# Kernel optimization log

Hardware: AMD Instinct MI355X
Metric: run time of the kernel (lower is better)

Reference implementation:

```python
import jax, jax.numpy as jnp
import numpy as np

N, E, F_IN, H, C = 50000, 800000, 128, 128, 64


def setup_inputs() -> dict:
    key = jax.random.key(0)
    ks = jax.random.split(key, 10)
    s = lambda f: np.float32(1.0 / np.sqrt(f))
    return {
        "x": jax.random.normal(ks[0], (N, F_IN), jnp.float32),
        "edge_index": jax.random.randint(ks[1], (2, E), 0, N, dtype=jnp.int64),
        # SAGEConv1: lin_l (on aggregated neighbors, with bias) + lin_r (on root, no bias)
        "W1l": jax.random.normal(ks[2], (F_IN, H), jnp.float32) * s(F_IN),
        "b1l": jnp.zeros((H,), jnp.float32),
        "W1r": jax.random.normal(ks[3], (F_IN, H), jnp.float32) * s(F_IN),
        # SAGEConv2
        "W2l": jax.random.normal(ks[4], (H, C), jnp.float32) * s(H),
        "b2l": jnp.zeros((C,), jnp.float32),
        "W2r": jax.random.normal(ks[5], (H, C), jnp.float32) * s(H),
        # GCNConv
        "Wg": jax.random.normal(ks[6], (C, C), jnp.float32) * s(C),
        "bg": jnp.zeros((C,), jnp.float32),
    }


def sage_conv(x, edge_index, Wl, bl, Wr):
    # PyG SAGEConv (mean aggr): out = lin_l(mean_{j in N(i)} x_j) + lin_r(x_i)
    n = x.shape[0]
    src, dst = edge_index[0], edge_index[1]
    agg = jax.ops.segment_sum(x[src], dst, num_segments=n)  # [N, F]
    cnt = jax.ops.segment_sum(jnp.ones((src.shape[0],), x.dtype), dst, num_segments=n)
    mean = agg / jnp.maximum(cnt, 1.0)[:, None]
    return mean @ Wl + bl + x @ Wr


def gcn_conv(x, edge_index, W, b):
    # PyG GCNConv: add self loops, symmetric normalization D^-1/2 A D^-1/2
    n = x.shape[0]
    loop = jnp.arange(n, dtype=edge_index.dtype)
    src = jnp.concatenate([edge_index[0], loop])
    dst = jnp.concatenate([edge_index[1], loop])
    deg = jax.ops.segment_sum(jnp.ones((src.shape[0],), x.dtype), dst, num_segments=n)
    dinv = jnp.where(deg > 0, jax.lax.rsqrt(jnp.maximum(deg, 1e-12)), 0.0)
    norm = dinv[src] * dinv[dst]  # [E+N]
    xw = x @ W
    out = jax.ops.segment_sum(xw[src] * norm[:, None], dst, num_segments=n)
    return out + b


def reference(x, edge_index, W1l, b1l, W1r, W2l, b2l, W2r, Wg, bg):
    h = jax.nn.relu(sage_conv(x, edge_index, W1l, b1l, W1r))
    # dropout is identity in eval mode
    h = sage_conv(h, edge_index, W2l, b2l, W2r)
    h = jax.nn.softmax(h, axis=1)  # activate='softmax'
    return gcn_conv(h, edge_index, Wg, bg)
```

## Files before the change

kernel.cpp:

```cpp
#include <hip/hip_runtime.h>
#include <hip/hip_fp16.h>
#include <math.h>


typedef __attribute__((ext_vector_type(8))) short bf16x8;
typedef __attribute__((ext_vector_type(4))) float f32x4;
typedef __attribute__((ext_vector_type(2))) float f32v2;

__device__ inline unsigned short f32_bf16_hi(float f) {
    unsigned int u = __builtin_bit_cast(unsigned int, f);
    u = (u + 0x7FFFu + ((u >> 16) & 1u)) >> 16;
    return (unsigned short)u;
}
__device__ inline float bf16_to_f32(unsigned short h) {
    unsigned int u = ((unsigned int)h) << 16;
    return __builtin_bit_cast(float, u);
}

union H8 { float4 f4; __half2 h[4]; };

__device__ inline void dec16(uint4 u, float* a0, float* a1) {
    f32v2 x0 = __builtin_amdgcn_cvt_pk_f32_fp8(u.x, false);
    f32v2 x1 = __builtin_amdgcn_cvt_pk_f32_fp8(u.x, true);
    f32v2 y0 = __builtin_amdgcn_cvt_pk_f32_fp8(u.y, false);
    f32v2 y1 = __builtin_amdgcn_cvt_pk_f32_fp8(u.y, true);
    a0[0] += x0[0]; a0[1] += x0[1]; a0[2] += x1[0]; a0[3] += x1[1];
    a0[4] += y0[0]; a0[5] += y0[1]; a0[6] += y1[0]; a0[7] += y1[1];
    f32v2 z0 = __builtin_amdgcn_cvt_pk_f32_fp8(u.z, false);
    f32v2 z1 = __builtin_amdgcn_cvt_pk_f32_fp8(u.z, true);
    f32v2 w0 = __builtin_amdgcn_cvt_pk_f32_fp8(u.w, false);
    f32v2 w1 = __builtin_amdgcn_cvt_pk_f32_fp8(u.w, true);
    a1[0] += z0[0]; a1[1] += z0[1]; a1[2] += z1[0]; a1[3] += z1[1];
    a1[4] += w0[0]; a1[5] += w0[1]; a1[6] += w1[0]; a1[7] += w1[1];
}

__global__ void count_kernel(const int* __restrict__ dst, int* __restrict__ off,
                             int E, int NB, int BK) {
    __shared__ int hist[256];
    int t = threadIdx.x;
    hist[t] = 0;
    __syncthreads();
    int base = blockIdx.x * 8192;
    for (int i = t; i < 8192; i += 256) {
        int e = base + i;
        if (e < E) atomicAdd(&hist[dst[e] >> 8], 1);
    }
    __syncthreads();
    if (t < BK) off[1 + t * NB + blockIdx.x] = hist[t];
    if (blockIdx.x == 0 && t == 0) off[0] = 0;
}

__global__ void scan_reduce_kernel(const int* __restrict__ data, int* __restrict__ bsum, int n) {
    __shared__ int red[256];
    int t = threadIdx.x;
    int base = blockIdx.x * 2048 + t * 8;
    int s = 0;
    if (base + 8 <= n) {
        int4 a = *(const int4*)(data + base);
        int4 b = *(const int4*)(data + base + 4);
        s = a.x + a.y + a.z + a.w + b.x + b.y + b.z + b.w;
    } else {
        for (int i = 0; i < 8; ++i)
            if (base + i < n) s += data[base + i];
    }
    red[t] = s;
    __syncthreads();
    for (int off = 128; off > 0; off >>= 1) {
        if (t < off) red[t] += red[t + off];
        __syncthreads();
    }
    if (t == 0) bsum[blockIdx.x] = red[0];
}

__global__ void scan_offsets_kernel(int* __restrict__ bsum, int B) {
    if (threadIdx.x == 0 && blockIdx.x == 0) {
        int run = 0;
        for (int i = 0; i < B; ++i) { int v = bsum[i]; bsum[i] = run; run += v; }
    }
}

__global__ void scan_final_kernel(int* __restrict__ data, const int* __restrict__ bsum, int n) {
    __shared__ int tsum[256];
    int t = threadIdx.x;
    int base = blockIdx.x * 2048 + t * 8;
    int v[8];
    int s = 0;
#pragma unroll
    for (int i = 0; i < 8; ++i) {
        v[i] = (base + i < n) ? data[base + i] : 0;
        s += v[i];
    }
    tsum[t] = s;
    for (int off = 1; off < 256; off <<= 1) {
        __syncthreads();
        int u = (t >= off) ? tsum[t - off] : 0;
        __syncthreads();
        tsum[t] += u;
    }
    __syncthreads();
    int run = bsum[blockIdx.x] + tsum[t] - s;
#pragma unroll
    for (int i = 0; i < 8; ++i) {
        run += v[i];
        if (base + i < n) data[base + i] = run;
    }
}

__global__ void partition_kernel(const int* __restrict__ src, const int* __restrict__ dst,
                                 const int* __restrict__ off, unsigned* __restrict__ ebuf,
                                 int E, int NB, int BK) {
    __shared__ int cur[256];
    int t = threadIdx.x;
    if (t < BK) cur[t] = off[t * NB + blockIdx.x];
    __syncthreads();
    int base = blockIdx.x * 8192;
    for (int i = t; i < 8192; i += 256) {
        int e = base + i;
        if (e < E) {
            int d = dst[e];
            int pos = atomicAdd(&cur[d >> 8], 1);
            ebuf[pos] = ((unsigned)src[e] << 8) | (unsigned)(d & 255);
        }
    }
}

__global__ void finalize_kernel(const unsigned* __restrict__ ebuf, const int* __restrict__ off,
                                int* __restrict__ col, int* __restrict__ rowptr,
                                float* __restrict__ dinv, int N, int NB, int E) {
    __shared__ int hist[256], scn[256], cur[256];
    int b = blockIdx.x, t = threadIdx.x;
    int base = off[b * NB];
    int end  = off[(b + 1) * NB];
    int M = end - base;
    hist[t] = 0;
    __syncthreads();
    for (int i = t; i < M; i += 256) atomicAdd(&hist[ebuf[base + i] & 255u], 1);
    __syncthreads();
    scn[t] = hist[t];
    for (int o = 1; o < 256; o <<= 1) {
        __syncthreads();
        int u = (t >= o) ? scn[t - o] : 0;
        __syncthreads();
        scn[t] += u;
    }
    __syncthreads();
    int excl = scn[t] - hist[t];
    int node = b * 256 + t;
    if (node < N) {
        rowptr[node] = base + excl;
        dinv[node] = rsqrtf((float)(hist[t] + 1));
    }
    if (b == 0 && t == 0) rowptr[N] = E;
    cur[t] = base + excl;
    __syncthreads();
    for (int i = t; i < M; i += 256) {
        unsigned w = ebuf[base + i];
        int pos = atomicAdd(&cur[w & 255u], 1);
        col[pos] = (int)(w >> 8);
    }
}

__global__ void packw_kernel(const float* __restrict__ W1l, const float* __restrict__ W1r,
                             const float* __restrict__ W2l, const float* __restrict__ W2r,
                             const float* __restrict__ Wg,
                             unsigned short* __restrict__ p1h, unsigned short* __restrict__ p1l,
                             unsigned short* __restrict__ p2h, unsigned short* __restrict__ p2l,
                             unsigned short* __restrict__ p3h, unsigned short* __restrict__ p3l) {
    int which = blockIdx.y;
    const float* W;
    unsigned short *hi, *lo;
    int K, Mp, colOff, T;
    if (which == 0)      { W = W1l; hi = p1h; lo = p1l; K = 128; Mp = 128; colOff = 0;   T = 16; }
    else if (which == 1) { W = W1r; hi = p1h; lo = p1l; K = 128; Mp = 128; colOff = 128; T = 16; }
    else if (which == 2) { W = W2l; hi = p2h; lo = p2l; K = 128; Mp = 64;  colOff = 0;   T = 8;  }
    else if (which == 3) { W = W2r; hi = p2h; lo = p2l; K = 128; Mp = 64;  colOff = 64;  T = 8;  }
    else                 { W = Wg;  hi = p3h; lo = p3l; K = 64;  Mp = 64;  colOff = 0;   T = 4;  }
    int idx = blockIdx.x * blockDim.x + threadIdx.x;
    if (idx >= K * Mp) return;
    int k = idx / Mp, m = idx % Mp;
    float w = W[(size_t)k * Mp + m];
    int colI = colOff + m;
    int s = k >> 5, kk = k & 31, qq = kk >> 3, j = kk & 7;
    int tt = colI >> 4, n = colI & 15;
    int lane = qq * 16 + n;
    size_t pos = ((size_t)(s * T + tt) * 64 + lane) * 8 + j;
    unsigned short h = f32_bf16_hi(w);
    hi[pos] = h;
    lo[pos] = f32_bf16_hi(w - bf16_to_f32(h));
}

__launch_bounds__(256)
__global__ void gemm1_kernel(const float* __restrict__ A,
                             const unsigned short* __restrict__ Whi,
                             const unsigned short* __restrict__ Wlo,
                             unsigned char* __restrict__ outA8, __half* __restrict__ outB, int N) {
    constexpr int Ttot = 16, TB = 8;
    __shared__ __align__(16) unsigned char pk[4][16][128];
    const int lane = threadIdx.x & 63;
    const int wave = threadIdx.x >> 6;
    const int m = lane & 15, q = lane >> 4;
    const int t0 = blockIdx.y * TB;
    const int row0 = blockIdx.x * 64 + wave * 16;
    int arow = row0 + m;
    if (arow >= N) arow = N - 1;
    const float* ap = A + (size_t)arow * 128 + q * 8;

    float av[4][8];
#pragma unroll
    for (int s = 0; s < 4; ++s) {
        *(float4*)(av[s])     = *(const float4*)(ap + s * 32);
        *(float4*)(av[s] + 4) = *(const float4*)(ap + s * 32 + 4);
    }
    bf16x8 ahi[4], alo[4];
#pragma unroll
    for (int s = 0; s < 4; ++s)
#pragma unroll
        for (int i = 0; i < 8; ++i) {
            unsigned short h = f32_bf16_hi(av[s][i]);
            ahi[s][i] = (short)h;
            alo[s][i] = (short)f32_bf16_hi(av[s][i] - bf16_to_f32(h));
        }

    f32x4 acc[TB];
#pragma unroll
    for (int t = 0; t < TB; ++t) acc[t] = (f32x4)(0.f);
    const bf16x8* whp = (const bf16x8*)Whi;
    const bf16x8* wlp = (const bf16x8*)Wlo;
#pragma unroll
    for (int s = 0; s < 4; ++s) {
        const int base = (s * Ttot + t0) * 64 + lane;
#pragma unroll
        for (int t = 0; t < TB; ++t) {
            bf16x8 wh = whp[base + t * 64];
            bf16x8 wl = wlp[base + t * 64];
            acc[t] = __builtin_amdgcn_mfma_f32_16x16x32_bf16(ahi[s], wh, acc[t], 0, 0, 0);
            acc[t] = __builtin_amdgcn_mfma_f32_16x16x32_bf16(alo[s], wh, acc[t], 0, 0, 0);
            acc[t] = __builtin_amdgcn_mfma_f32_16x16x32_bf16(ahi[s], wl, acc[t], 0, 0, 0);
        }
    }

    if (blockIdx.y == 0) {
#pragma unroll
        for (int r = 0; r < 4; ++r) {
            int row = q * 4 + r;
            int sw = (row & 3) << 5;
#pragma unroll
            for (int t = 0; t < 8; t += 2) {
                int w = __builtin_amdgcn_cvt_pk_fp8_f32(acc[t][r], acc[t + 1][r], 0, false);
                int off = (t >> 1) * 8 + (m & 7);
                int c0 = ((2 * t + (m >> 3)) & 3) * 32 + off;
                int c1 = ((2 * t + 2 + (m >> 3)) & 3) * 32 + off;
                pk[wave][row][c0 ^ sw] = (unsigned char)(w & 0xff);
                pk[wave][row][c1 ^ sw] = (unsigned char)((w >> 8) & 0xff);
            }
        }
        __syncthreads();
        int rr = lane >> 2, qt = lane & 3;
        int grow = row0 + rr;
        if (grow < N) {
            const unsigned char* srcp = &pk[wave][rr][(qt ^ (rr & 3)) * 32];
            uint4 v0 = *(const uint4*)(srcp);
            uint4 v1 = *(const uint4*)(srcp + 16);
            *(uint4*)(outA8 + (size_t)grow * 128 + qt * 32) = v0;
            *(uint4*)(outA8 + (size_t)grow * 128 + qt * 32 + 16) = v1;
        }
    } else {
#pragma unroll
        for (int r = 0; r < 4; ++r) {
            int row = row0 + q * 4 + r;
            if (row < N) {
#pragma unroll
                for (int t = 0; t < TB; ++t) {
                    int c = (t0 + t) * 16 + m - 128;
                    outB[(size_t)row * 128 + c] = __float2half(acc[t][r]);
                }
            }
        }
    }
}

__launch_bounds__(256)
__global__ void sage2_fused_kernel(const unsigned char* __restrict__ p8, const __half* __restrict__ q16,
                                   const int* __restrict__ rowptr, const int* __restrict__ col,
                                   const float* __restrict__ b1l,
                                   const unsigned short* __restrict__ Whi,
                                   const unsigned short* __restrict__ Wlo,
                                   __half* __restrict__ r16, __half* __restrict__ s16, int N) {
    __shared__ float part[4][64][16];
    const int lane = threadIdx.x & 63;
    const int w = threadIdx.x >> 6;
    const int m = lane & 15, q = lane >> 4;
    const int row0 = blockIdx.x * 16;
    int node = row0 + m;
    int nclamp = (node < N) ? node : (N - 1);
    int sAll = rowptr[nclamp];
    int eAll = (node < N) ? rowptr[nclamp + 1] : sAll;
    int deg  = eAll - sAll;
    int sIdx = sAll + ((deg * w) >> 2);
    int eIdx = sAll + ((deg * (w + 1)) >> 2);

    float acc[4][8];
#pragma unroll
    for (int s = 0; s < 4; ++s)
#pragma unroll
        for (int i = 0; i < 8; ++i) acc[s][i] = 0.f;

    const unsigned char* pb = p8 + q * 32;
    int ptr = sIdx;
    for (; ptr + 4 <= eIdx; ptr += 4) {
        int j0 = col[ptr], j1 = col[ptr + 1], j2 = col[ptr + 2], j3 = col[ptr + 3];
        uint4 uA[4], uB[4];
        uA[0] = *(const uint4*)(pb + (size_t)j0 * 128);
        uB[0] = *(const uint4*)(pb + (size_t)j0 * 128 + 16);
        uA[1] = *(const uint4*)(pb + (size_t)j1 * 128);
        uB[1] = *(const uint4*)(pb + (size_t)j1 * 128 + 16);
        uA[2] = *(const uint4*)(pb + (size_t)j2 * 128);
        uB[2] = *(const uint4*)(pb + (size_t)j2 * 128 + 16);
        uA[3] = *(const uint4*)(pb + (size_t)j3 * 128);
        uB[3] = *(const uint4*)(pb + (size_t)j3 * 128 + 16);
#pragma unroll
        for (int e = 0; e < 4; ++e) {
            dec16(uA[e], acc[0], acc[1]);
            dec16(uB[e], acc[2], acc[3]);
        }
    }
    for (; ptr < eIdx; ++ptr) {
        int j0 = col[ptr];
        uint4 uA = *(const uint4*)(pb + (size_t)j0 * 128);
        uint4 uB = *(const uint4*)(pb + (size_t)j0 * 128 + 16);
        dec16(uA, acc[0], acc[1]);
        dec16(uB, acc[2], acc[3]);
    }

    float* ap = &acc[0][0];
    const int swz = lane & 3;
#pragma unroll
    for (int c = 0; c < 2; ++c) {
        if (c) __syncthreads();
#pragma unroll
        for (int sl = 0; sl < 4; ++sl)
            *(float4*)&part[w][lane][(sl ^ swz) * 4] =
                *(const float4*)(ap + (c * 4 + sl) * 4);
        __syncthreads();
#pragma unroll
        for (int p = 1; p < 4; ++p) {
#pragma unroll
            for (int sl = 0; sl < 4; ++sl) {
                float4 pv = *(const float4*)&part[w ^ p][lane][(sl ^ swz) * 4];
                int g = (c * 4 + sl) * 4;
                ap[g]     += pv.x;
                ap[g + 1] += pv.y;
                ap[g + 2] += pv.z;
                ap[g + 3] += pv.w;
            }
        }
    }

    float inv = 1.0f / fmaxf((float)deg, 1.0f);
    bf16x8 ahi[4], alo[4];
#pragma unroll
    for (int s = 0; s < 4; ++s) {
        H8 qv;
        qv.f4 = *(const float4*)(q16 + (size_t)nclamp * 128 + s * 32 + q * 8);
        float bv[8];
        *(float4*)(bv)     = *(const float4*)(b1l + s * 32 + q * 8);
        *(float4*)(bv + 4) = *(const float4*)(b1l + s * 32 + q * 8 + 4);
#pragma unroll
        for (int i = 0; i < 8; ++i) {
            float qf = __half2float(((const __half*)&qv)[i]);
            float h = fmaxf(acc[s][i] * inv + qf + bv[i], 0.f);
            unsigned short hb = f32_bf16_hi(h);
            ahi[s][i] = (short)hb;
            alo[s][i] = (short)f32_bf16_hi(h - bf16_to_f32(hb));
        }
    }

    f32x4 accm[2];
#pragma unroll
    for (int t = 0; t < 2; ++t) accm[t] = (f32x4)(0.f);
    const bf16x8* whp = (const bf16x8*)Whi;
    const bf16x8* wlp = (const bf16x8*)Wlo;
#pragma unroll
    for (int s = 0; s < 4; ++s) {
        const int base = (s * 8 + 2 * w) * 64 + lane;
#pragma unroll
        for (int t = 0; t < 2; ++t) {
            bf16x8 wh = whp[base + t * 64];
            bf16x8 wl = wlp[base + t * 64];
            accm[t] = __builtin_amdgcn_mfma_f32_16x16x32_bf16(ahi[s], wh, accm[t], 0, 0, 0);
            accm[t] = __builtin_amdgcn_mfma_f32_16x16x32_bf16(alo[s], wh, accm[t], 0, 0, 0);
            accm[t] = __builtin_amdgcn_mfma_f32_16x16x32_bf16(ahi[s], wl, accm[t], 0, 0, 0);
        }
    }
    __half* op = (w >= 2) ? s16 : r16;
#pragma unroll
    for (int r = 0; r < 4; ++r) {
        int row = row0 + q * 4 + r;
        if (row < N) {
#pragma unroll
            for (int t = 0; t < 2; ++t) {
                int c = ((2 * w + t) * 16 + m) & 63;
                op[(size_t)row * 64 + c] = __float2half(accm[t][r]);
            }
        }
    }
}

__launch_bounds__(256)
__global__ void gcn_prep_fused_kernel(const __half* __restrict__ r16, const __half* __restrict__ s16,
                                      const int* __restrict__ rowptr, const int* __restrict__ col,
                                      const float* __restrict__ b2l,
                                      const unsigned short* __restrict__ Whi,
                                      const unsigned short* __restrict__ Wlo,
                                      const float* __restrict__ dinv,
                                      __half* __restrict__ tp16, int N) {
    __shared__ float part[4][64][16];
    const int lane = threadIdx.x & 63;
    const int w = threadIdx.x >> 6;
    const int m = lane & 15, q = lane >> 4;
    const int row0 = blockIdx.x * 16;
    int node = row0 + m;
    int nclamp = (node < N) ? node : (N - 1);
    int sAll = rowptr[nclamp];
    int eAll = (node < N) ? rowptr[nclamp + 1] : sAll;
    int deg  = eAll - sAll;
    int sIdx = sAll + ((deg * w) >> 2);
    int eIdx = sAll + ((deg * (w + 1)) >> 2);

    float acc[2][8];
#pragma unroll
    for (int s = 0; s < 2; ++s)
#pragma unroll
        for (int i = 0; i < 8; ++i) acc[s][i] = 0.f;

    const __half* rb = r16 + q * 8;
    int ptr = sIdx;
    for (; ptr + 4 <= eIdx; ptr += 4) {
        int j0 = col[ptr], j1 = col[ptr + 1], j2 = col[ptr + 2], j3 = col[ptr + 3];
        H8 u[4][2];
#pragma unroll
        for (int s = 0; s < 2; ++s) {
            u[0][s].f4 = *(const float4*)(rb + (size_t)j0 * 64 + s * 32);
            u[1][s].f4 = *(const float4*)(rb + (size_t)j1 * 64 + s * 32);
            u[2][s].f4 = *(const float4*)(rb + (size_t)j2 * 64 + s * 32);
            u[3][s].f4 = *(const float4*)(rb + (size_t)j3 * 64 + s * 32);
        }
#pragma unroll
        for (int s = 0; s < 2; ++s)
#pragma unroll
            for (int k = 0; k < 4; ++k) {
                float2 f0 = __half22float2(u[0][s].h[k]);
                float2 f1 = __half22float2(u[1][s].h[k]);
                float2 f2 = __half22float2(u[2][s].h[k]);
                float2 f3 = __half22float2(u[3][s].h[k]);
                acc[s][2 * k]     += (f0.x + f1.x) + (f2.x + f3.x);
                acc[s][2 * k + 1] += (f0.y + f1.y) + (f2.y + f3.y);
            }
    }
    for (; ptr < eIdx; ++ptr) {
        int j0 = col[ptr];
#pragma unroll
        for (int s = 0; s < 2; ++s) {
            H8 u0;
            u0.f4 = *(const float4*)(rb + (size_t)j0 * 64 + s * 32);
#pragma unroll
            for (int k = 0; k < 4; ++k) {
                float2 f0 = __half22float2(u0.h[k]);
                acc[s][2 * k]     += f0.x;
                acc[s][2 * k + 1] += f0.y;
            }
        }
    }

    float* ap = &acc[0][0];
    const int swz = lane & 3;
#pragma unroll
    for (int sl = 0; sl < 4; ++sl)
        *(float4*)&part[w][lane][(sl ^ swz) * 4] = *(const float4*)(ap + sl * 4);
    __syncthreads();
#pragma unroll
    for (int p = 1; p < 4; ++p) {
#pragma unroll
        for (int sl = 0; sl < 4; ++sl) {
            float4 pv = *(const float4*)&part[w ^ p][lane][(sl ^ swz) * 4];
            ap[sl * 4]     += pv.x;
            ap[sl * 4 + 1] += pv.y;
            ap[sl * 4 + 2] += pv.z;
            ap[sl * 4 + 3] += pv.w;
        }
    }

    float inv = 1.0f / fmaxf((float)deg, 1.0f);
    float v[2][8];
    float mx = -1e30f;
#pragma unroll
    for (int s = 0; s < 2; ++s) {
        H8 sv;
        sv.f4 = *(const float4*)(s16 + (size_t)nclamp * 64 + s * 32 + q * 8);
        float bv[8];
        *(float4*)(bv)     = *(const float4*)(b2l + s * 32 + q * 8);
        *(float4*)(bv + 4) = *(const float4*)(b2l + s * 32 + q * 8 + 4);
#pragma unroll
        for (int i = 0; i < 8; ++i) {
            float sf = __half2float(((const __half*)&sv)[i]);
            v[s][i] = acc[s][i] * inv + sf + bv[i];
            mx = fmaxf(mx, v[s][i]);
        }
    }
    mx = fmaxf(mx, __shfl_xor(mx, 16, 64));
    mx = fmaxf(mx, __shfl_xor(mx, 32, 64));
    float sm = 0.f;
#pragma unroll
    for (int s = 0; s < 2; ++s)
#pragma unroll
        for (int i = 0; i < 8; ++i) {
            v[s][i] = expf(v[s][i] - mx);
            sm += v[s][i];
        }
    sm += __shfl_xor(sm, 16, 64);
    sm += __shfl_xor(sm, 32, 64);
    float is = 1.0f / sm;

    bf16x8 ahi[2], alo[2];
#pragma unroll
    for (int s = 0; s < 2; ++s)
#pragma unroll
        for (int i = 0; i < 8; ++i) {
            float h = v[s][i] * is;
            unsigned short hb = f32_bf16_hi(h);
            ahi[s][i] = (short)hb;
            alo[s][i] = (short)f32_bf16_hi(h - bf16_to_f32(hb));
        }

    f32x4 accm = (f32x4)(0.f);
    const bf16x8* whp = (const bf16x8*)Whi;
    const bf16x8* wlp = (const bf16x8*)Wlo;
#pragma unroll
    for (int s = 0; s < 2; ++s) {
        const int base = (s * 4 + w) * 64 + lane;
        bf16x8 wh = whp[base];
        bf16x8 wl = wlp[base];
        accm = __builtin_amdgcn_mfma_f32_16x16x32_bf16(ahi[s], wh, accm, 0, 0, 0);
        accm = __builtin_amdgcn_mfma_f32_16x16x32_bf16(alo[s], wh, accm, 0, 0, 0);
        accm = __builtin_amdgcn_mfma_f32_16x16x32_bf16(ahi[s], wl, accm, 0, 0, 0);
    }
#pragma unroll
    for (int r = 0; r < 4; ++r) {
        int row = row0 + q * 4 + r;
        if (row < N) {
            float sc = dinv[row];
            int c = w * 16 + m;
            tp16[(size_t)row * 64 + c] = __float2half(accm[r] * sc);
        }
    }
}

__global__ void gcn_agg_kernel(const __half* __restrict__ tp,
                               const int* __restrict__ rowptr, const int* __restrict__ col,
                               const float* __restrict__ dinv, const float* __restrict__ bg,
                               float* __restrict__ out, int N) {
    int node = blockIdx.x * 4 + (threadIdx.x >> 6);
    if (node >= N) return;
    int lane = threadIdx.x & 63;
    int f2 = lane & 31;
    int ep = lane >> 5;
    int s = rowptr[node], e = rowptr[node + 1];
    float ax[8], ay[8];
#pragma unroll
    for (int k = 0; k < 8; ++k) { ax[k] = 0.f; ay[k] = 0.f; }
    int p = s;
    for (; p + 16 <= e; p += 16) {
#pragma unroll
        for (int k = 0; k < 8; ++k) {
            int j = col[p + 2 * k + ep];
            float2 f = __half22float2(*(const __half2*)(tp + (size_t)j * 64 + 2 * f2));
            ax[k] += f.x;
            ay[k] += f.y;
        }
    }
    for (int t = p + ep; t < e; t += 2) {
        int j = col[t];
        float2 f = __half22float2(*(const __half2*)(tp + (size_t)j * 64 + 2 * f2));
        ax[0] += f.x;
        ay[0] += f.y;
    }
    float sx = ((ax[0] + ax[1]) + (ax[2] + ax[3])) + ((ax[4] + ax[5]) + (ax[6] + ax[7]));
    float sy = ((ay[0] + ay[1]) + (ay[2] + ay[3])) + ((ay[4] + ay[5]) + (ay[6] + ay[7]));
    sx += __shfl_xor(sx, 32, 64);
    sy += __shfl_xor(sy, 32, 64);
    if (ep == 0) {
        float2 selfv = __half22float2(*(const __half2*)(tp + (size_t)node * 64 + 2 * f2));
        float di = dinv[node];
        float2 o;
        o.x = (sx + selfv.x) * di + bg[2 * f2];
        o.y = (sy + selfv.y) * di + bg[2 * f2 + 1];
        *(float2*)(out + (size_t)node * 64 + 2 * f2) = o;
    }
}

extern "C" void kernel_launch(void* const* d_in, const int* in_sizes, int n_in,
                              void* d_out, int out_size, void* d_ws, size_t ws_size,
                              hipStream_t stream) {
    const float* x = (const float*)d_in[0];
    const int* ei = (const int*)d_in[1];
    const float* W1l = (const float*)d_in[2];
    const float* b1l = (const float*)d_in[3];
    const float* W1r = (const float*)d_in[4];
    const float* W2l = (const float*)d_in[5];
    const float* b2l = (const float*)d_in[6];
    const float* W2r = (const float*)d_in[7];
    const float* Wg  = (const float*)d_in[8];
    const float* bg  = (const float*)d_in[9];

    const int N = in_sizes[0] / 128;
    const int E = in_sizes[1] / 2;
    const int* srcp = ei;
    const int* dstp = ei + E;

    const int NB = (E + 8191) / 8192;
    const int BK = (N + 255) >> 8;
    const int len = BK * NB;

    float* ws = (float*)d_ws;
    float* dinv = ws;
    unsigned char* p8 = (unsigned char*)(dinv + N);
    __half* q16 = (__half*)(p8 + (size_t)N * 128);
    __half* r16 = q16 + (size_t)N * 128;
    __half* s16 = r16 + (size_t)N * 64;
    __half* tp16 = s16 + (size_t)N * 64;
    int* rowptr = (int*)(tp16 + (size_t)N * 64);
    int* off    = rowptr + (N + 1);
    int* colbuf = off + len + 2;
    unsigned* ebuf = (unsigned*)(colbuf + E);
    int* bsum   = (int*)(ebuf + E);
    uintptr_t up = (uintptr_t)(bsum + 32);
    up = (up + 15) & ~(uintptr_t)15;
    unsigned short* p1h = (unsigned short*)up;
    unsigned short* p1l = p1h + 32768;
    unsigned short* p2h = p1l + 32768;
    unsigned short* p2l = p2h + 16384;
    unsigned short* p3h = p2l + 16384;
    unsigned short* p3l = p3h + 4096;

    float* out = (float*)d_out;

    count_kernel<<<NB, 256, 0, stream>>>(dstp, off, E, NB, BK);
    const int sn = len + 1;
    const int SBs = (sn + 2047) / 2048;
    scan_reduce_kernel<<<SBs, 256, 0, stream>>>(off, bsum, sn);
    scan_offsets_kernel<<<1, 64, 0, stream>>>(bsum, SBs);
    scan_final_kernel<<<SBs, 256, 0, stream>>>(off, bsum, sn);
    partition_kernel<<<NB, 256, 0, stream>>>(srcp, dstp, off, ebuf, E, NB, BK);
    finalize_kernel<<<BK, 256, 0, stream>>>(ebuf, off, colbuf, rowptr, dinv, N, NB, E);

    packw_kernel<<<dim3(64, 5), 256, 0, stream>>>(W1l, W1r, W2l, W2r, Wg,
                                                  p1h, p1l, p2h, p2l, p3h, p3l);

    const int gb  = (N + 63) / 64;
    const int gbf = (N + 15) / 16;
    const int ab  = (N + 3) / 4;

    gemm1_kernel<<<dim3(gb, 2), 256, 0, stream>>>(x, p1h, p1l, p8, q16, N);

    sage2_fused_kernel<<<gbf, 256, 0, stream>>>(p8, q16, rowptr, colbuf, b1l,
                                                p2h, p2l, r16, s16, N);

    gcn_prep_fused_kernel<<<gbf, 256, 0, stream>>>(r16, s16, rowptr, colbuf, b2l,
                                                   p3h, p3l, dinv, tp16, N);

    gcn_agg_kernel<<<ab, 256, 0, stream>>>(tp16, rowptr, colbuf, dinv, bg, out, N);
}
```

Before: 277.3 us.

## Store sage2 neighbor projection in fp8, split waves into pairs, and split GCN aggregation by feature half

The sage2 projection r, which gcn_prep gathers per edge, is now stored as fp8 instead of fp16, halving the bytes gathered in the second aggregation. Both fused kernels now process 32 rows per block with wave pairs splitting each node's edges, instead of 16 rows with four waves splitting edges. Each wave pair computes the full 64-column output for its rows. GCN output is written as two 32-column half planes, and the final aggregation runs as two launches so each gather touches a smaller row footprint. fp8 storage of r adds quantization error to the second SAGE layer's aggregated term.

```diff
diff --git a/kernel.cpp b/kernel.cpp
--- a/kernel.cpp
+++ b/kernel.cpp
@@ -32,6 +32,11 @@
     f32v2 w1 = __builtin_amdgcn_cvt_pk_f32_fp8(u.w, true);
     a1[0] += z0[0]; a1[1] += z0[1]; a1[2] += z1[0]; a1[3] += z1[1];
     a1[4] += w0[0]; a1[5] += w0[1]; a1[6] += w1[0]; a1[7] += w1[1];
+}
+
+__device__ inline unsigned char enc8(float v) {
+    int w = __builtin_amdgcn_cvt_pk_fp8_f32(v, v, 0, false);
+    return (unsigned char)(w & 0xff);
 }
 
 __global__ void count_kernel(const int* __restrict__ dst, int* __restrict__ off,
@@ -285,19 +290,22 @@
                                    const float* __restrict__ b1l,
                                    const unsigned short* __restrict__ Whi,
                                    const unsigned short* __restrict__ Wlo,
-                                   __half* __restrict__ r16, __half* __restrict__ s16, int N) {
+                                   unsigned char* __restrict__ r8, __half* __restrict__ s16, int N) {
     __shared__ float part[4][64][16];
     const int lane = threadIdx.x & 63;
-    const int w = threadIdx.x >> 6;
+    const int wave = threadIdx.x >> 6;
+    const int pairH = wave & 1;
+    const int grp   = wave >> 1;
     const int m = lane & 15, q = lane >> 4;
-    const int row0 = blockIdx.x * 16;
+    const int row0 = blockIdx.x * 32 + grp * 16;
     int node = row0 + m;
     int nclamp = (node < N) ? node : (N - 1);
     int sAll = rowptr[nclamp];
     int eAll = (node < N) ? rowptr[nclamp + 1] : sAll;
     int deg  = eAll - sAll;
-    int sIdx = sAll + ((deg * w) >> 2);
-    int eIdx = sAll + ((deg * (w + 1)) >> 2);
+    int half0 = (deg + 1) >> 1;
+    int sIdx = sAll + (pairH ? half0 : 0);
+    int eIdx = pairH ? eAll : (sAll + half0);
 
     float acc[4][8];
 #pragma unroll
@@ -339,20 +347,17 @@
         if (c) __syncthreads();
 #pragma unroll
         for (int sl = 0; sl < 4; ++sl)
-            *(float4*)&part[w][lane][(sl ^ swz) * 4] =
+            *(float4*)&part[wave][lane][(sl ^ swz) * 4] =
                 *(const float4*)(ap + (c * 4 + sl) * 4);
         __syncthreads();
 #pragma unroll
-        for (int p = 1; p < 4; ++p) {
-#pragma unroll
-            for (int sl = 0; sl < 4; ++sl) {
-                float4 pv = *(const float4*)&part[w ^ p][lane][(sl ^ swz) * 4];
-                int g = (c * 4 + sl) * 4;
-                ap[g]     += pv.x;
-                ap[g + 1] += pv.y;
-                ap[g + 2] += pv.z;
-                ap[g + 3] += pv.w;
-            }
+        for (int sl = 0; sl < 4; ++sl) {
+            float4 pv = *(const float4*)&part[wave ^ 1][lane][(sl ^ swz) * 4];
+            int g = (c * 4 + sl) * 4;
+            ap[g]     += pv.x;
+            ap[g + 1] += pv.y;
+            ap[g + 2] += pv.z;
+            ap[g + 3] += pv.w;
         }
     }
 
@@ -375,14 +380,159 @@
         }
     }
 
+    f32x4 accm[4];
+#pragma unroll
+    for (int t = 0; t < 4; ++t) accm[t] = (f32x4)(0.f);
+    const bf16x8* whp = (const bf16x8*)Whi;
+    const bf16x8* wlp = (const bf16x8*)Wlo;
+#pragma unroll
+    for (int s = 0; s < 4; ++s) {
+        const int base = (s * 8 + pairH * 4) * 64 + lane;
+#pragma unroll
+        for (int t = 0; t < 4; ++t) {
+            bf16x8 wh = whp[base + t * 64];
+            bf16x8 wl = wlp[base + t * 64];
+            accm[t] = __builtin_amdgcn_mfma_f32_16x16x32_bf16(ahi[s], wh, accm[t], 0, 0, 0);
+            accm[t] = __builtin_amdgcn_mfma_f32_16x16x32_bf16(alo[s], wh, accm[t], 0, 0, 0);
+            accm[t] = __builtin_amdgcn_mfma_f32_16x16x32_bf16(ahi[s], wl, accm[t], 0, 0, 0);
+        }
+    }
+#pragma unroll
+    for (int r = 0; r < 4; ++r) {
+        int row = row0 + q * 4 + r;
+        if (row < N) {
+            if (pairH == 0) {
+#pragma unroll
+                for (int t = 0; t < 4; ++t) {
+                    int c = t * 16 + m;
+                    int pos = ((c >> 3) & 3) * 16 + ((c >> 5) & 1) * 8 + (c & 7);
+                    r8[(size_t)row * 64 + pos] = enc8(accm[t][r]);
+                }
+            } else {
+#pragma unroll
+                for (int t = 0; t < 4; ++t) {
+                    int c = t * 16 + m;
+                    s16[(size_t)row * 64 + c] = __float2half(accm[t][r]);
+                }
+            }
+        }
+    }
+}
+
+__launch_bounds__(256)
+__global__ void gcn_prep_fused_kernel(const unsigned char* __restrict__ r8, const __half* __restrict__ s16,
+                                      const int* __restrict__ rowptr, const int* __restrict__ col,
+                                      const float* __restrict__ b2l,
+                                      const unsigned short* __restrict__ Whi,
+                                      const unsigned short* __restrict__ Wlo,
+                                      const float* __restrict__ dinv,
+                                      __half* __restrict__ tpA, __half* __restrict__ tpB, int N) {
+    __shared__ float part[4][64][16];
+    const int lane = threadIdx.x & 63;
+    const int wave = threadIdx.x >> 6;
+    const int pairH = wave & 1;
+    const int grp   = wave >> 1;
+    const int m = lane & 15, q = lane >> 4;
+    const int row0 = blockIdx.x * 32 + grp * 16;
+    int node = row0 + m;
+    int nclamp = (node < N) ? node : (N - 1);
+    int sAll = rowptr[nclamp];
+    int eAll = (node < N) ? rowptr[nclamp + 1] : sAll;
+    int deg  = eAll - sAll;
+    int half0 = (deg + 1) >> 1;
+    int sIdx = sAll + (pairH ? half0 : 0);
+    int eIdx = pairH ? eAll : (sAll + half0);
+
+    float acc[2][8];
+#pragma unroll
+    for (int s = 0; s < 2; ++s)
+#pragma unroll
+        for (int i = 0; i < 8; ++i) acc[s][i] = 0.f;
+
+    const unsigned char* rb = r8 + q * 16;
+    int ptr = sIdx;
+    for (; ptr + 4 <= eIdx; ptr += 4) {
+        int j0 = col[ptr], j1 = col[ptr + 1], j2 = col[ptr + 2], j3 = col[ptr + 3];
+        uint4 u0 = *(const uint4*)(rb + (size_t)j0 * 64);
+        uint4 u1 = *(const uint4*)(rb + (size_t)j1 * 64);
+        uint4 u2 = *(const uint4*)(rb + (size_t)j2 * 64);
+        uint4 u3 = *(const uint4*)(rb + (size_t)j3 * 64);
+        dec16(u0, acc[0], acc[1]);
+        dec16(u1, acc[0], acc[1]);
+        dec16(u2, acc[0], acc[1]);
+        dec16(u3, acc[0], acc[1]);
+    }
+    for (; ptr < eIdx; ++ptr) {
+        int j0 = col[ptr];
+        uint4 u0 = *(const uint4*)(rb + (size_t)j0 * 64);
+        dec16(u0, acc[0], acc[1]);
+    }
+
+    float* ap = &acc[0][0];
+    const int swz = lane & 3;
+#pragma unroll
+    for (int sl = 0; sl < 4; ++sl)
+        *(float4*)&part[wave][lane][(sl ^ swz) * 4] = *(const float4*)(ap + sl * 4);
+    __syncthreads();
+#pragma unroll
+    for (int sl = 0; sl < 4; ++sl) {
+        float4 pv = *(const float4*)&part[wave ^ 1][lane][(sl ^ swz) * 4];
+        ap[sl * 4]     += pv.x;
+        ap[sl * 4 + 1] += pv.y;
+        ap[sl * 4 + 2] += pv.z;
+        ap[sl * 4 + 3] += pv.w;
+    }
+
+    float inv = 1.0f / fmaxf((float)deg, 1.0f);
+    float v[2][8];
+    float mx = -1e30f;
+#pragma unroll
+    for (int s = 0; s < 2; ++s) {
+        H8 sv;
+        sv.f4 = *(const float4*)(s16 + (size_t)nclamp * 64 + s * 32 + q * 8);
+        float bv[8];
+        *(float4*)(bv)     = *(const float4*)(b2l + s * 32 + q * 8);
+        *(float4*)(bv + 4) = *(const float4*)(b2l + s * 32 + q * 8 + 4);
+#pragma unroll
+        for (int i = 0; i < 8; ++i) {
+            float sf = __half2float(((const __half*)&sv)[i]);
+            v[s][i] = acc[s][i] * inv + sf + bv[i];
+            mx = fmaxf(mx, v[s][i]);
+        }
+    }
+    mx = fmaxf(mx, __shfl_xor(mx, 16, 64));
+    mx = fmaxf(mx, __shfl_xor(mx, 32, 64));
+    float sm = 0.f;
+#pragma unroll
+    for (int s = 0; s < 2; ++s)
+#pragma unroll
+        for (int i = 0; i < 8; ++i) {
+            v[s][i] = expf(v[s][i] - mx);
+            sm += v[s][i];
+        }
+    sm += __shfl_xor(sm, 16, 64);
+    sm += __shfl_xor(sm, 32, 64);
+    float is = 1.0f / sm;
+
+    bf16x8 ahi[2], alo[2];
+#pragma unroll
+    for (int s = 0; s < 2; ++s)
+#pragma unroll
+        for (int i = 0; i < 8; ++i) {
+            float h = v[s][i] * is;
+            unsigned short hb = f32_bf16_hi(h);
+            ahi[s][i] = (short)hb;
+            alo[s][i] = (short)f32_bf16_hi(h - bf16_to_f32(hb));
+        }
+
     f32x4 accm[2];
 #pragma unroll
     for (int t = 0; t < 2; ++t) accm[t] = (f32x4)(0.f);
     const bf16x8* whp = (const bf16x8*)Whi;
     const bf16x8* wlp = (const bf16x8*)Wlo;
 #pragma unroll
-    for (int s = 0; s < 4; ++s) {
-        const int base = (s * 8 + 2 * w) * 64 + lane;
+    for (int s = 0; s < 2; ++s) {
+        const int base = (s * 4 + pairH * 2) * 64 + lane;
 #pragma unroll
         for (int t = 0; t < 2; ++t) {
             bf16x8 wh = whp[base + t * 64];
@@ -392,209 +542,61 @@
             accm[t] = __builtin_amdgcn_mfma_f32_16x16x32_bf16(ahi[s], wl, accm[t], 0, 0, 0);
         }
     }
-    __half* op = (w >= 2) ? s16 : r16;
-#pragma unroll
-    for (int r = 0; r < 4; ++r) {
-        int row = row0 + q * 4 + r;
-        if (row < N) {
-#pragma unroll
-            for (int t = 0; t < 2; ++t) {
-                int c = ((2 * w + t) * 16 + m) & 63;
-                op[(size_t)row * 64 + c] = __float2half(accm[t][r]);
-            }
-        }
-    }
-}
-
-__launch_bounds__(256)
-__global__ void gcn_prep_fused_kernel(const __half* __restrict__ r16, const __half* __restrict__ s16,
-                                      const int* __restrict__ rowptr, const int* __restrict__ col,
-                                      const float* __restrict__ b2l,
-                                      const unsigned short* __restrict__ Whi,
-                                      const unsigned short* __restrict__ Wlo,
-                                      const float* __restrict__ dinv,
-                                      __half* __restrict__ tp16, int N) {
-    __shared__ float part[4][64][16];
-    const int lane = threadIdx.x & 63;
-    const int w = threadIdx.x >> 6;
-    const int m = lane & 15, q = lane >> 4;
-    const int row0 = blockIdx.x * 16;
-    int node = row0 + m;
-    int nclamp = (node < N) ? node : (N - 1);
-    int sAll = rowptr[nclamp];
-    int eAll = (node < N) ? rowptr[nclamp + 1] : sAll;
-    int deg  = eAll - sAll;
-    int sIdx = sAll + ((deg * w) >> 2);
-    int eIdx = sAll + ((deg * (w + 1)) >> 2);
-
-    float acc[2][8];
-#pragma unroll
-    for (int s = 0; s < 2; ++s)
-#pragma unroll
-        for (int i = 0; i < 8; ++i) acc[s][i] = 0.f;
-
-    const __half* rb = r16 + q * 8;
-    int ptr = sIdx;
-    for (; ptr + 4 <= eIdx; ptr += 4) {
-        int j0 = col[ptr], j1 = col[ptr + 1], j2 = col[ptr + 2], j3 = col[ptr + 3];
-        H8 u[4][2];
-#pragma unroll
-        for (int s = 0; s < 2; ++s) {
-            u[0][s].f4 = *(const float4*)(rb + (size_t)j0 * 64 + s * 32);
-            u[1][s].f4 = *(const float4*)(rb + (size_t)j1 * 64 + s * 32);
-            u[2][s].f4 = *(const float4*)(rb + (size_t)j2 * 64 + s * 32);
-            u[3][s].f4 = *(const float4*)(rb + (size_t)j3 * 64 + s * 32);
-        }
-#pragma unroll
-        for (int s = 0; s < 2; ++s)
-#pragma unroll
-            for (int k = 0; k < 4; ++k) {
-                float2 f0 = __half22float2(u[0][s].h[k]);
-                float2 f1 = __half22float2(u[1][s].h[k]);
-                float2 f2 = __half22float2(u[2][s].h[k]);
-                float2 f3 = __half22float2(u[3][s].h[k]);
-                acc[s][2 * k]     += (f0.x + f1.x) + (f2.x + f3.x);
-                acc[s][2 * k + 1] += (f0.y + f1.y) + (f2.y + f3.y);
-            }
-    }
-    for (; ptr < eIdx; ++ptr) {
-        int j0 = col[ptr];
-#pragma unroll
-        for (int s = 0; s < 2; ++s) {
-            H8 u0;
-            u0.f4 = *(const float4*)(rb + (size_t)j0 * 64 + s * 32);
-#pragma unroll
-            for (int k = 0; k < 4; ++k) {
-                float2 f0 = __half22float2(u0.h[k]);
-                acc[s][2 * k]     += f0.x;
-                acc[s][2 * k + 1] += f0.y;
-            }
-        }
-    }
-
-    float* ap = &acc[0][0];
-    const int swz = lane & 3;
-#pragma unroll
-    for (int sl = 0; sl < 4; ++sl)
-        *(float4*)&part[w][lane][(sl ^ swz) * 4] = *(const float4*)(ap + sl * 4);
-    __syncthreads();
-#pragma unroll
-    for (int p = 1; p < 4; ++p) {
-#pragma unroll
-        for (int sl = 0; sl < 4; ++sl) {
-            float4 pv = *(const float4*)&part[w ^ p][lane][(sl ^ swz) * 4];
-            ap[sl * 4]     += pv.x;
-            ap[sl * 4 + 1] += pv.y;
-            ap[sl * 4 + 2] += pv.z;
-            ap[sl * 4 + 3] += pv.w;
-        }
-    }
-
-    float inv = 1.0f / fmaxf((float)deg, 1.0f);
-    float v[2][8];
-    float mx = -1e30f;
-#pragma unroll
-    for (int s = 0; s < 2; ++s) {
-        H8 sv;
-        sv.f4 = *(const float4*)(s16 + (size_t)nclamp * 64 + s * 32 + q * 8);
-        float bv[8];
-        *(float4*)(bv)     = *(const float4*)(b2l + s * 32 + q * 8);
-        *(float4*)(bv + 4) = *(const float4*)(b2l + s * 32 + q * 8 + 4);
-#pragma unroll
-        for (int i = 0; i < 8; ++i) {
-            float sf = __half2float(((const __half*)&sv)[i]);
-            v[s][i] = acc[s][i] * inv + sf + bv[i];
-            mx = fmaxf(mx, v[s][i]);
-        }
-    }
-    mx = fmaxf(mx, __shfl_xor(mx, 16, 64));
-    mx = fmaxf(mx, __shfl_xor(mx, 32, 64));
-    float sm = 0.f;
-#pragma unroll
-    for (int s = 0; s < 2; ++s)
-#pragma unroll
-        for (int i = 0; i < 8; ++i) {
-            v[s][i] = expf(v[s][i] - mx);
-            sm += v[s][i];
-        }
-    sm += __shfl_xor(sm, 16, 64);
-    sm += __shfl_xor(sm, 32, 64);
-    float is = 1.0f / sm;
-
-    bf16x8 ahi[2], alo[2];
-#pragma unroll
-    for (int s = 0; s < 2; ++s)
-#pragma unroll
-        for (int i = 0; i < 8; ++i) {
-            float h = v[s][i] * is;
-            unsigned short hb = f32_bf16_hi(h);
-            ahi[s][i] = (short)hb;
-            alo[s][i] = (short)f32_bf16_hi(h - bf16_to_f32(hb));
-        }
-
-    f32x4 accm = (f32x4)(0.f);
-    const bf16x8* whp = (const bf16x8*)Whi;
-    const bf16x8* wlp = (const bf16x8*)Wlo;
-#pragma unroll
-    for (int s = 0; s < 2; ++s) {
-        const int base = (s * 4 + w) * 64 + lane;
-        bf16x8 wh = whp[base];
-        bf16x8 wl = wlp[base];
-        accm = __builtin_amdgcn_mfma_f32_16x16x32_bf16(ahi[s], wh, accm, 0, 0, 0);
-        accm = __builtin_amdgcn_mfma_f32_16x16x32_bf16(alo[s], wh, accm, 0, 0, 0);
-        accm = __builtin_amdgcn_mfma_f32_16x16x32_bf16(ahi[s], wl, accm, 0, 0, 0);
-    }
+    __half* plane = pairH ? tpB : tpA;
 #pragma unroll
     for (int r = 0; r < 4; ++r) {
         int row = row0 + q * 4 + r;
         if (row < N) {
             float sc = dinv[row];
-            int c = w * 16 + m;
-            tp16[(size_t)row * 64 + c] = __float2half(accm[r] * sc);
-        }
-    }
-}
-
-__global__ void gcn_agg_kernel(const __half* __restrict__ tp,
+#pragma unroll
+            for (int t = 0; t < 2; ++t) {
+                int c = t * 16 + m;
+                plane[(size_t)row * 32 + c] = __float2half(accm[t][r] * sc);
+            }
+        }
+    }
+}
+
+__global__ void gcn_agg_kernel(const __half* __restrict__ tpP,
                                const int* __restrict__ rowptr, const int* __restrict__ col,
                                const float* __restrict__ dinv, const float* __restrict__ bg,
-                               float* __restrict__ out, int N) {
+                               float* __restrict__ out, int N, int fOff) {
     int node = blockIdx.x * 4 + (threadIdx.x >> 6);
     if (node >= N) return;
     int lane = threadIdx.x & 63;
-    int f2 = lane & 31;
-    int ep = lane >> 5;
+    int f2 = lane & 15;
+    int ep = lane >> 4;
     int s = rowptr[node], e = rowptr[node + 1];
-    float ax[8], ay[8];
-#pragma unroll
-    for (int k = 0; k < 8; ++k) { ax[k] = 0.f; ay[k] = 0.f; }
+    float ax[4], ay[4];
+#pragma unroll
+    for (int k = 0; k < 4; ++k) { ax[k] = 0.f; ay[k] = 0.f; }
     int p = s;
     for (; p + 16 <= e; p += 16) {
 #pragma unroll
-        for (int k = 0; k < 8; ++k) {
-            int j = col[p + 2 * k + ep];
-            float2 f = __half22float2(*(const __half2*)(tp + (size_t)j * 64 + 2 * f2));
+        for (int k = 0; k < 4; ++k) {
+            int j = col[p + 4 * k + ep];
+            float2 f = __half22float2(*(const __half2*)(tpP + (size_t)j * 32 + 2 * f2));
             ax[k] += f.x;
             ay[k] += f.y;
         }
     }
-    for (int t = p + ep; t < e; t += 2) {
+    for (int t = p + ep; t < e; t += 4) {
         int j = col[t];
-        float2 f = __half22float2(*(const __half2*)(tp + (size_t)j * 64 + 2 * f2));
+        float2 f = __half22float2(*(const __half2*)(tpP + (size_t)j * 32 + 2 * f2));
         ax[0] += f.x;
         ay[0] += f.y;
     }
-    float sx = ((ax[0] + ax[1]) + (ax[2] + ax[3])) + ((ax[4] + ax[5]) + (ax[6] + ax[7]));
-    float sy = ((ay[0] + ay[1]) + (ay[2] + ay[3])) + ((ay[4] + ay[5]) + (ay[6] + ay[7]));
-    sx += __shfl_xor(sx, 32, 64);
-    sy += __shfl_xor(sy, 32, 64);
+    float sx = (ax[0] + ax[1]) + (ax[2] + ax[3]);
+    float sy = (ay[0] + ay[1]) + (ay[2] + ay[3]);
+    sx += __shfl_xor(sx, 16, 64); sx += __shfl_xor(sx, 32, 64);
+    sy += __shfl_xor(sy, 16, 64); sy += __shfl_xor(sy, 32, 64);
     if (ep == 0) {
-        float2 selfv = __half22float2(*(const __half2*)(tp + (size_t)node * 64 + 2 * f2));
+        float2 selfv = __half22float2(*(const __half2*)(tpP + (size_t)node * 32 + 2 * f2));
         float di = dinv[node];
         float2 o;
-        o.x = (sx + selfv.x) * di + bg[2 * f2];
-        o.y = (sy + selfv.y) * di + bg[2 * f2 + 1];
-        *(float2*)(out + (size_t)node * 64 + 2 * f2) = o;
+        o.x = (sx + selfv.x) * di + bg[fOff + 2 * f2];
+        o.y = (sy + selfv.y) * di + bg[fOff + 2 * f2 + 1];
+        *(float2*)(out + (size_t)node * 64 + fOff + 2 * f2) = o;
     }
 }
 
@@ -625,10 +627,11 @@
     float* dinv = ws;
     unsigned char* p8 = (unsigned char*)(dinv + N);
     __half* q16 = (__half*)(p8 + (size_t)N * 128);
-    __half* r16 = q16 + (size_t)N * 128;
-    __half* s16 = r16 + (size_t)N * 64;
-    __half* tp16 = s16 + (size_t)N * 64;
-    int* rowptr = (int*)(tp16 + (size_t)N * 64);
+    unsigned char* r8 = (unsigned char*)(q16 + (size_t)N * 128);
+    __half* s16 = (__half*)(r8 + (size_t)N * 64);
+    __half* tpA = s16 + (size_t)N * 64;
+    __half* tpB = tpA + (size_t)N * 32;
+    int* rowptr = (int*)(tpB + (size_t)N * 32);
     int* off    = rowptr + (N + 1);
     int* colbuf = off + len + 2;
     unsigned* ebuf = (unsigned*)(colbuf + E);
@@ -657,16 +660,17 @@
                                                   p1h, p1l, p2h, p2l, p3h, p3l);
 
     const int gb  = (N + 63) / 64;
-    const int gbf = (N + 15) / 16;
+    const int gbf = (N + 31) / 32;
     const int ab  = (N + 3) / 4;
 
     gemm1_kernel<<<dim3(gb, 2), 256, 0, stream>>>(x, p1h, p1l, p8, q16, N);
 
     sage2_fused_kernel<<<gbf, 256, 0, stream>>>(p8, q16, rowptr, colbuf, b1l,
-                                                p2h, p2l, r16, s16, N);
-
-    gcn_prep_fused_kernel<<<gbf, 256, 0, stream>>>(r16, s16, rowptr, colbuf, b2l,
-                                                   p3h, p3l, dinv, tp16, N);
-
-    gcn_agg_kernel<<<ab, 256, 0, stream>>>(tp16, rowptr, colbuf, dinv, bg, out, N);
-}
+                                                p2h, p2l, r8, s16, N);
+
+    gcn_prep_fused_kernel<<<gbf, 256, 0, stream>>>(r8, s16, rowptr, colbuf, b2l,
+                                                   p3h, p3l, dinv, tpA, tpB, N);
+
+    gcn_agg_kernel<<<ab, 256, 0, stream>>>(tpA, rowptr, colbuf, dinv, bg, out, N, 0);
+    gcn_agg_kernel<<<ab, 256, 0, stream>>>(tpB, rowptr, colbuf, dinv, bg, out, N, 32);
+}
```

Result: faster. 271.4 us (-2.1%).
